# Performance work log

Hardware: AMD Instinct MI355X
Metric: run time of the kernel (lower is better)

Reference implementation:

```python
import jax, jax.numpy as jnp
import numpy as np

BETA = 0.25
K = 1024   # num_codebook_vectors
D = 256    # latent_dim


def setup_inputs() -> dict:
    key = jax.random.key(0)
    k1, k2 = jax.random.split(key)
    z = jax.random.normal(k1, (32, D, 32, 32), dtype=jnp.float32)
    # original init: uniform(-1/K, 1/K)
    codebook = jax.random.uniform(k2, (K, D), dtype=jnp.float32, minval=-1.0 / K, maxval=1.0 / K)
    return {"z": z, "codebook": codebook}


def reference(z, codebook):
    B, C, H, W = z.shape
    sg = jax.lax.stop_gradient
    # NCHW -> NHWC, flatten to [N, D]
    z_nhwc = jnp.transpose(z, (0, 2, 3, 1))
    zf = z_nhwc.reshape(-1, C)
    # squared distances via sum-of-squares + matmul: [N, K]
    d = (jnp.sum(zf * zf, axis=1, keepdims=True)
         + jnp.sum(codebook * codebook, axis=1)
         - 2.0 * jnp.matmul(zf, codebook.T))
    idx = jnp.argmin(d, axis=1)                      # [N]
    z_q = codebook[idx].reshape(B, H, W, C)          # gather + reshape
    # commitment + codebook loss
    loss = (jnp.mean((sg(z_q) - z_nhwc) ** 2)
            + BETA * jnp.mean((z_q - sg(z_nhwc)) ** 2))
    # straight-through estimator
    z_q = z_nhwc + sg(z_q - z_nhwc)
    z_q = jnp.transpose(z_q, (0, 3, 1, 2))           # back to NCHW
    return z_q, idx, loss
```

## Files before the change

kernel.cpp:

```cpp
#include <hip/hip_runtime.h>

constexpr int D_ = 256;
constexpr int K_ = 1024;
constexpr int P_ = 1024;
constexpr int N_ = 32768;

constexpr int IDX_OFF  = 8388608;
constexpr int LOSS_OFF = 8421376;

constexpr int CB16_OFF = 0;
constexpr int CN_OFF   = 262400;
constexpr int ZN_OFF   = 263424;
constexpr int CNT_OFF  = 296448;
constexpr int WL_OFF   = 296449;
constexpr size_t SCRATCH_BYTES = (size_t)(WL_OFF + N_) * 4;

constexpr float RESCUE_MARGIN = 1e-4f;

typedef _Float16 half8 __attribute__((ext_vector_type(8)));
typedef float f32x4 __attribute__((ext_vector_type(4)));

__device__ __forceinline__ void stage16(const float* g, float* l) {
  __builtin_amdgcn_global_load_lds(
      (const __attribute__((address_space(1))) unsigned int*)g,
      (__attribute__((address_space(3))) unsigned int*)l, 16, 0, 0);
}

__global__ __launch_bounds__(64) void vq_prep(const float* __restrict__ z,
                                              const float* __restrict__ cb,
                                              float* __restrict__ scratch,
                                              float* __restrict__ loss) {
  const int blk = blockIdx.x;
  const int lane = threadIdx.x;
  if (blk < 512) {
    const int n0 = blk * 64;
    const int b = n0 >> 10, p0 = n0 & (P_ - 1);
    const float* zp = z + (size_t)b * (D_ * P_) + p0 + lane;
    float a8[8];
    #pragma unroll
    for (int i = 0; i < 8; ++i) a8[i] = 0.0f;
    for (int oct = 0; oct < 32; ++oct) {
      #pragma unroll
      for (int i = 0; i < 8; ++i) {
        float v = zp[(size_t)(oct * 8 + i) * P_];
        a8[i] = fmaf(v, v, a8[i]);
      }
    }
    scratch[ZN_OFF + n0 + lane] = ((a8[0] + a8[1]) + (a8[2] + a8[3])) +
                                  ((a8[4] + a8[5]) + (a8[6] + a8[7]));
    if (blk == 0 && lane == 0) {
      *loss = 0.0f;
      ((int*)(scratch + CNT_OFF))[0] = 0;
    }
  } else if (blk < 1536) {
    const int k = blk - 512;
    const float* row = cb + (size_t)k * D_;
    double s = 0.0;
    #pragma unroll
    for (int i = 0; i < 4; ++i) {
      double v = (double)row[lane + i * 64];
      s = fma(v, v, s);
    }
    #pragma unroll
    for (int off = 32; off; off >>= 1) s += __shfl_down(s, off, 64);
    if (lane == 0) scratch[CN_OFF + k] = (float)s;
  } else {
    const int kt = blk - 1536;
    const int k = kt * 16 + (lane & 15);
    const int quad = lane >> 4;
    _Float16* cw = (_Float16*)(scratch + CB16_OFF);
    for (int ds = 0; ds < 8; ++ds) {
      const float* src = cb + (size_t)k * D_ + ds * 32 + quad * 8;
      half8 h, lo;
      #pragma unroll
      for (int j = 0; j < 8; ++j) {
        const float v = src[j] * 1024.0f;
        const _Float16 hh = (_Float16)v;
        h[j] = hh;
        lo[j] = (_Float16)(v - (float)hh);
      }
      const int s = kt * 8 + ds;
      *(half8*)(cw + ((size_t)(s * 2 + 0) * 64 + lane) * 8) = h;
      *(half8*)(cw + ((size_t)(s * 2 + 1) * 64 + lane) * 8) = lo;
    }
  }
}

__global__ __launch_bounds__(256, 2) void vq_mfma(const float* __restrict__ z,
                                                  const float* __restrict__ scratch_c,
                                                  float* __restrict__ scratch,
                                                  float* __restrict__ idxf) {
  const int t = threadIdx.x;
  const int w = t >> 6;
  const int l = t & 63;
  const int quad = l >> 4;
  const int col = l & 15;
  const int rh = w & 1;
  const int cs = w >> 1;
  const int n0 = blockIdx.x * 64;
  const int b = n0 >> 10;
  const int p0 = n0 & (P_ - 1);

  const float* __restrict__ cbsw_f = scratch_c + CB16_OFF;
  const float* __restrict__ cnorm = scratch_c + CN_OFF;
  const float* __restrict__ zn = scratch_c + ZN_OFF;

  __shared__ alignas(16) float Bw[4][2][2048];
  __shared__ alignas(16) float cnLds[1024];
  __shared__ float sM1[4][32];
  __shared__ float sM2[4][32];
  __shared__ int   sI1[4][32];
  float* Azs = &Bw[0][0][0];

  *(float4*)(cnLds + t * 4) = *(const float4*)(cnorm + t * 4);

  float znr[2][4];
  #pragma unroll
  for (int rt = 0; rt < 2; ++rt) {
    const float4 znv = *(const float4*)(zn + n0 + rh * 32 + rt * 16 + quad * 4);
    znr[rt][0] = znv.x; znr[rt][1] = znv.y;
    znr[rt][2] = znv.z; znr[rt][3] = znv.w;
  }

  half8 Ah[2][8], Al[2][8];
  const int dl0 = w * 8;
  for (int ds = 0; ds < 8; ++ds) {
    __syncthreads();
    #pragma unroll
    for (int i = 0; i < 8; ++i) {
      const int dloc = dl0 + i;
      Azs[l * 33 + dloc] =
          z[(size_t)b * (D_ * P_) + (size_t)(ds * 32 + dloc) * P_ + p0 + l];
    }
    __syncthreads();
    #pragma unroll
    for (int rt = 0; rt < 2; ++rt) {
      const float* src = &Azs[(rh * 32 + rt * 16 + col) * 33 + quad * 8];
      half8 h, lo;
      #pragma unroll
      for (int j = 0; j < 8; ++j) {
        const float v = src[j];
        const _Float16 hh = (_Float16)v;
        h[j] = hh;
        lo[j] = (_Float16)(v - (float)hh);
      }
      Ah[rt][ds] = h;
      Al[rt][ds] = lo;
    }
  }
  __syncthreads();
  asm volatile("s_waitcnt vmcnt(0)" ::: "memory");

  float* myb0 = &Bw[w][0][0];
  float* myb1 = &Bw[w][1][0];
  const float* gs = cbsw_f + (size_t)cs * 32 * 4096 + l * 4;

  #pragma unroll
  for (int j = 0; j < 8; ++j) stage16(gs + j * 256, myb0 + j * 256);

  float m1[2][4], m2v[2][4];
  int i1[2][4];
  #pragma unroll
  for (int rt = 0; rt < 2; ++rt)
    #pragma unroll
    for (int r = 0; r < 4; ++r) { m1[rt][r] = 1e30f; m2v[rt][r] = 1e30f; i1[rt][r] = 0; }

  const float* cnp = cnLds + cs * 512 + col;
  int kg = cs * 512 + col;

  for (int kt = 0; kt < 32; ++kt) {
    f32x4 H0 = {0.f,0.f,0.f,0.f}, M0 = {0.f,0.f,0.f,0.f}, L0 = {0.f,0.f,0.f,0.f};
    f32x4 H1 = {0.f,0.f,0.f,0.f}, M1 = {0.f,0.f,0.f,0.f}, L1 = {0.f,0.f,0.f,0.f};

    {
      const float* gsp = gs + (size_t)(kt * 2 + 1) * 2048;
      #pragma unroll
      for (int j = 0; j < 8; ++j) stage16(gsp + j * 256, myb1 + j * 256);
      asm volatile("s_waitcnt vmcnt(8)" ::: "memory");
      __builtin_amdgcn_sched_barrier(0);

      __builtin_amdgcn_s_setprio(1);
      #pragma unroll
      for (int ds = 0; ds < 4; ++ds) {
        const half8 bh = *(const half8*)(myb0 + (ds * 2 + 0) * 256 + l * 4);
        const half8 bl = *(const half8*)(myb0 + (ds * 2 + 1) * 256 + l * 4);
        H0 = __builtin_amdgcn_mfma_f32_16x16x32_f16(Ah[0][ds], bh, H0, 0, 0, 0);
        H1 = __builtin_amdgcn_mfma_f32_16x16x32_f16(Ah[1][ds], bh, H1, 0, 0, 0);
        M0 = __builtin_amdgcn_mfma_f32_16x16x32_f16(Ah[0][ds], bl, M0, 0, 0, 0);
        M1 = __builtin_amdgcn_mfma_f32_16x16x32_f16(Ah[1][ds], bl, M1, 0, 0, 0);
        L0 = __builtin_amdgcn_mfma_f32_16x16x32_f16(Al[0][ds], bh, L0, 0, 0, 0);
        L1 = __builtin_amdgcn_mfma_f32_16x16x32_f16(Al[1][ds], bh, L1, 0, 0, 0);
      }
      __builtin_amdgcn_s_setprio(0);
    }

    {
      if (kt < 31) {
        const float* gsp = gs + (size_t)(kt * 2 + 2) * 2048;
        #pragma unroll
        for (int j = 0; j < 8; ++j) stage16(gsp + j * 256, myb0 + j * 256);
        asm volatile("s_waitcnt vmcnt(8)" ::: "memory");
      } else {
        asm volatile("s_waitcnt vmcnt(0)" ::: "memory");
      }
      __builtin_amdgcn_sched_barrier(0);

      __builtin_amdgcn_s_setprio(1);
      #pragma unroll
      for (int ds = 4; ds < 8; ++ds) {
        const half8 bh = *(const half8*)(myb1 + ((ds - 4) * 2 + 0) * 256 + l * 4);
        const half8 bl = *(const half8*)(myb1 + ((ds - 4) * 2 + 1) * 256 + l * 4);
        H0 = __builtin_amdgcn_mfma_f32_16x16x32_f16(Ah[0][ds], bh, H0, 0, 0, 0);
        H1 = __builtin_amdgcn_mfma_f32_16x16x32_f16(Ah[1][ds], bh, H1, 0, 0, 0);
        M0 = __builtin_amdgcn_mfma_f32_16x16x32_f16(Ah[0][ds], bl, M0, 0, 0, 0);
        M1 = __builtin_amdgcn_mfma_f32_16x16x32_f16(Ah[1][ds], bl, M1, 0, 0, 0);
        L0 = __builtin_amdgcn_mfma_f32_16x16x32_f16(Al[0][ds], bh, L0, 0, 0, 0);
        L1 = __builtin_amdgcn_mfma_f32_16x16x32_f16(Al[1][ds], bh, L1, 0, 0, 0);
      }
      __builtin_amdgcn_s_setprio(0);

      const float cnf = *cnp;
      #pragma unroll
      for (int r = 0; r < 4; ++r) {
        const float s0 = fmaf((H0[r] + M0[r]) + L0[r], -0x1p-9f, znr[0][r] + cnf);
        if (s0 < m1[0][r]) { m2v[0][r] = m1[0][r]; m1[0][r] = s0; i1[0][r] = kg; }
        else if (s0 < m2v[0][r]) m2v[0][r] = s0;
        const float s1 = fmaf((H1[r] + M1[r]) + L1[r], -0x1p-9f, znr[1][r] + cnf);
        if (s1 < m1[1][r]) { m2v[1][r] = m1[1][r]; m1[1][r] = s1; i1[1][r] = kg; }
        else if (s1 < m2v[1][r]) m2v[1][r] = s1;
      }
      cnp += 16;
      kg += 16;
    }
  }

  #pragma unroll
  for (int off = 1; off <= 8; off <<= 1) {
    #pragma unroll
    for (int rt = 0; rt < 2; ++rt)
      #pragma unroll
      for (int r = 0; r < 4; ++r) {
        const float o1 = __shfl_xor(m1[rt][r], off, 64);
        const float o2 = __shfl_xor(m2v[rt][r], off, 64);
        const int oi = __shfl_xor(i1[rt][r], off, 64);
        if (o1 < m1[rt][r]) { m2v[rt][r] = fminf(m1[rt][r], o2); m1[rt][r] = o1; i1[rt][r] = oi; }
        else if (o1 == m1[rt][r]) { i1[rt][r] = min(i1[rt][r], oi); m2v[rt][r] = m1[rt][r]; }
        else { m2v[rt][r] = fminf(m2v[rt][r], o1); }
      }
  }

  if (col == 0) {
    #pragma unroll
    for (int rt = 0; rt < 2; ++rt)
      #pragma unroll
      for (int r = 0; r < 4; ++r) {
        const int rl = rt * 16 + quad * 4 + r;
        sM1[w][rl] = m1[rt][r];
        sM2[w][rl] = m2v[rt][r];
        sI1[w][rl] = i1[rt][r];
      }
  }
  __syncthreads();
  if (w < 2 && col == 0) {
    int* cnt = (int*)(scratch + CNT_OFF);
    int* wl = (int*)(scratch + WL_OFF);
    #pragma unroll
    for (int rt = 0; rt < 2; ++rt)
      #pragma unroll
      for (int r = 0; r < 4; ++r) {
        const int rl = rt * 16 + quad * 4 + r;
        float a1 = sM1[w][rl], a2 = sM2[w][rl];
        int ai = sI1[w][rl];
        const float o1 = sM1[w + 2][rl], o2 = sM2[w + 2][rl];
        const int oi = sI1[w + 2][rl];
        if (o1 < a1) { a2 = fminf(a1, o2); a1 = o1; ai = oi; }
        else if (o1 == a1) { ai = min(ai, oi); a2 = a1; }
        else { a2 = fminf(a2, o1); }
        const int n = n0 + w * 32 + rl;
        idxf[n] = (float)ai;
        if (a2 - a1 < RESCUE_MARGIN) {
          const int pos = atomicAdd(cnt, 1);
          wl[pos] = n;
        }
      }
  }
}

__global__ __launch_bounds__(256, 4) void vq_rescue(const float* __restrict__ z,
                                                    const float* __restrict__ cb,
                                                    const float* __restrict__ scratch,
                                                    float* __restrict__ idxf) {
  const int tid = threadIdx.x;
  const float* cnorm = scratch + CN_OFF;
  const float* zn = scratch + ZN_OFF;
  const int count = ((const int*)(scratch + CNT_OFF))[0];
  const int* wl = (const int*)(scratch + WL_OFF);

  __shared__ alignas(16) float zb[8][D_];
  __shared__ int nrow[8];
  __shared__ float rv[256];
  __shared__ int ri[256];

  for (int base = blockIdx.x * 8; base < count; base += gridDim.x * 8) {
    const int take = min(8, count - base);
    if (tid < 8) nrow[tid] = wl[base + (tid < take ? tid : 0)];
    __syncthreads();
    #pragma unroll
    for (int r = 0; r < 8; ++r) {
      const int n = nrow[r];
      const int b = n >> 10, p = n & (P_ - 1);
      zb[r][tid] = z[(size_t)b * (D_ * P_) + (size_t)tid * P_ + p];
    }
    __syncthreads();

    const int k0 = tid * 4;
    const float4* __restrict__ cr0 = (const float4*)(cb + (size_t)(k0 + 0) * D_);
    const float4* __restrict__ cr1 = (const float4*)(cb + (size_t)(k0 + 1) * D_);
    const float4* __restrict__ cr2 = (const float4*)(cb + (size_t)(k0 + 2) * D_);
    const float4* __restrict__ cr3 = (const float4*)(cb + (size_t)(k0 + 3) * D_);

    float acc[8][4];
    #pragma unroll
    for (int r = 0; r < 8; ++r)
      #pragma unroll
      for (int j = 0; j < 4; ++j) acc[r][j] = 0.0f;

    for (int d4 = 0; d4 < 64; ++d4) {
      const float4 v0 = cr0[d4], v1 = cr1[d4], v2 = cr2[d4], v3 = cr3[d4];
      #pragma unroll
      for (int r = 0; r < 8; ++r) {
        const float4 zv = ((const float4*)zb[r])[d4];
        acc[r][0] = fmaf(zv.x, v0.x, acc[r][0]);
        acc[r][0] = fmaf(zv.y, v0.y, acc[r][0]);
        acc[r][0] = fmaf(zv.z, v0.z, acc[r][0]);
        acc[r][0] = fmaf(zv.w, v0.w, acc[r][0]);
        acc[r][1] = fmaf(zv.x, v1.x, acc[r][1]);
        acc[r][1] = fmaf(zv.y, v1.y, acc[r][1]);
        acc[r][1] = fmaf(zv.z, v1.z, acc[r][1]);
        acc[r][1] = fmaf(zv.w, v1.w, acc[r][1]);
        acc[r][2] = fmaf(zv.x, v2.x, acc[r][2]);
        acc[r][2] = fmaf(zv.y, v2.y, acc[r][2]);
        acc[r][2] = fmaf(zv.z, v2.z, acc[r][2]);
        acc[r][2] = fmaf(zv.w, v2.w, acc[r][2]);
        acc[r][3] = fmaf(zv.x, v3.x, acc[r][3]);
        acc[r][3] = fmaf(zv.y, v3.y, acc[r][3]);
        acc[r][3] = fmaf(zv.z, v3.z, acc[r][3]);
        acc[r][3] = fmaf(zv.w, v3.w, acc[r][3]);
      }
    }

    for (int r = 0; r < 8; ++r) {
      const int n = nrow[r];
      const float zA = zn[n];
      float bv = 1e30f;
      int bi = 0x7fffffff;
      #pragma unroll
      for (int j = 0; j < 4; ++j) {
        const float A = zA + cnorm[k0 + j];
        const float s = A - 2.0f * acc[r][j];
        if (s < bv) { bv = s; bi = k0 + j; }
      }
      rv[tid] = bv; ri[tid] = bi;
      __syncthreads();
      for (int off = 128; off >= 1; off >>= 1) {
        if (tid < off) {
          const float ov = rv[tid + off];
          const int oi = ri[tid + off];
          if (ov < rv[tid] || (ov == rv[tid] && oi < ri[tid])) { rv[tid] = ov; ri[tid] = oi; }
        }
        __syncthreads();
      }
      if (tid == 0 && r < take) idxf[n] = (float)ri[0];
      __syncthreads();
    }
  }
}

__global__ __launch_bounds__(256) void vq_gather(const float* __restrict__ z,
                                                 const float* __restrict__ cb,
                                                 const float* __restrict__ idxf,
                                                 float* __restrict__ out,
                                                 float* __restrict__ loss) {
  const int tid = threadIdx.x;
  const int lane = tid & 63;
  const int w = tid >> 6;
  const int n0 = blockIdx.x * 64;
  const int b = n0 >> 10;
  const int p0 = n0 & (P_ - 1);
  const int p = p0 + lane;

  const int idx = (int)(idxf[n0 + lane] + 0.5f);
  const float4* crow4 = (const float4*)(cb + (size_t)idx * D_);
  const size_t base = (size_t)b * (D_ * P_) + p;

  float acc = 0.0f;
  #pragma unroll 4
  for (int ci = 0; ci < 16; ++ci) {
    const float4 v = crow4[w * 16 + ci];
    const int c = w * 64 + ci * 4;
    const float vv[4] = {v.x, v.y, v.z, v.w};
    #pragma unroll
    for (int u = 0; u < 4; ++u) {
      const size_t a = base + (size_t)(c + u) * P_;
      const float zv = z[a];
      const float d = vv[u] - zv;
      out[a] = zv + d;
      acc = fmaf(d, d, acc);
    }
  }
  #pragma unroll
  for (int off = 32; off; off >>= 1) acc += __shfl_down(acc, off, 64);
  __shared__ float wsum[4];
  if (lane == 0) wsum[w] = acc;
  __syncthreads();
  if (tid == 0) {
    float s = wsum[0] + wsum[1] + wsum[2] + wsum[3];
    atomicAdd(loss, s * (1.25f / 8388608.0f));
  }
}

extern "C" void kernel_launch(void* const* d_in, const int* in_sizes, int n_in,
                              void* d_out, int out_size, void* d_ws, size_t ws_size,
                              hipStream_t stream) {
  const float* z = (const float*)d_in[0];
  const float* cb = (const float*)d_in[1];
  float* out = (float*)d_out;

  float* scratch = (d_ws != nullptr && ws_size >= SCRATCH_BYTES)
                       ? (float*)d_ws : out;

  vq_prep<<<1600, 64, 0, stream>>>(z, cb, scratch, out + LOSS_OFF);
  vq_mfma<<<N_ / 64, 256, 0, stream>>>(z, scratch, scratch, out + IDX_OFF);
  vq_rescue<<<128, 256, 0, stream>>>(z, cb, scratch, out + IDX_OFF);
  vq_gather<<<N_ / 64, 256, 0, stream>>>(z, cb, out + IDX_OFF, out, out + LOSS_OFF);
}
```

Before: 234.9 us.

## Split codebook across eight waves per block with finer double-buffered staging

The distance/argmin kernel now uses 512 threads (8 waves) per block, and each wave pair covers 256 codebook entries instead of 512. Codebook staging into LDS moves to quarter-size chunks that are double-buffered with a vmcnt(4) wait. The final cross-wave reduction merges four partial top-2 results per row instead of two. The aim is more waves in flight to hide latency and halve per-wave serial work, at the cost of more registers per CU under the tighter launch bounds and extra reduction and synchronisation overhead.

```diff
diff --git a/kernel.cpp b/kernel.cpp
--- a/kernel.cpp
+++ b/kernel.cpp
@@ -86,7 +86,7 @@
   }
 }
 
-__global__ __launch_bounds__(256, 2) void vq_mfma(const float* __restrict__ z,
+__global__ __launch_bounds__(512, 4) void vq_mfma(const float* __restrict__ z,
                                                   const float* __restrict__ scratch_c,
                                                   float* __restrict__ scratch,
                                                   float* __restrict__ idxf) {
@@ -105,14 +105,14 @@
   const float* __restrict__ cnorm = scratch_c + CN_OFF;
   const float* __restrict__ zn = scratch_c + ZN_OFF;
 
-  __shared__ alignas(16) float Bw[4][2][2048];
+  __shared__ alignas(16) float Bw[8][2][1024];
   __shared__ alignas(16) float cnLds[1024];
-  __shared__ float sM1[4][32];
-  __shared__ float sM2[4][32];
-  __shared__ int   sI1[4][32];
+  __shared__ float sM1[8][32];
+  __shared__ float sM2[8][32];
+  __shared__ int   sI1[8][32];
   float* Azs = &Bw[0][0][0];
 
-  *(float4*)(cnLds + t * 4) = *(const float4*)(cnorm + t * 4);
+  *(float2*)(cnLds + t * 2) = *(const float2*)(cnorm + t * 2);
 
   float znr[2][4];
   #pragma unroll
@@ -123,11 +123,11 @@
   }
 
   half8 Ah[2][8], Al[2][8];
-  const int dl0 = w * 8;
+  const int dl0 = w * 4;
   for (int ds = 0; ds < 8; ++ds) {
     __syncthreads();
     #pragma unroll
-    for (int i = 0; i < 8; ++i) {
+    for (int i = 0; i < 4; ++i) {
       const int dloc = dl0 + i;
       Azs[l * 33 + dloc] =
           z[(size_t)b * (D_ * P_) + (size_t)(ds * 32 + dloc) * P_ + p0 + l];
@@ -151,12 +151,12 @@
   __syncthreads();
   asm volatile("s_waitcnt vmcnt(0)" ::: "memory");
 
-  float* myb0 = &Bw[w][0][0];
-  float* myb1 = &Bw[w][1][0];
-  const float* gs = cbsw_f + (size_t)cs * 32 * 4096 + l * 4;
+  float* myq0 = &Bw[w][0][0];
+  float* myq1 = &Bw[w][1][0];
+  const float* gs = cbsw_f + (size_t)cs * 16 * 4096 + l * 4;
 
   #pragma unroll
-  for (int j = 0; j < 8; ++j) stage16(gs + j * 256, myb0 + j * 256);
+  for (int j = 0; j < 4; ++j) stage16(gs + j * 256, myq0 + j * 256);
 
   float m1[2][4], m2v[2][4];
   int i1[2][4];
@@ -165,25 +165,34 @@
     #pragma unroll
     for (int r = 0; r < 4; ++r) { m1[rt][r] = 1e30f; m2v[rt][r] = 1e30f; i1[rt][r] = 0; }
 
-  const float* cnp = cnLds + cs * 512 + col;
-  int kg = cs * 512 + col;
-
-  for (int kt = 0; kt < 32; ++kt) {
+  const float* cnp = cnLds + cs * 256 + col;
+  int kg = cs * 256 + col;
+
+  for (int kt = 0; kt < 16; ++kt) {
     f32x4 H0 = {0.f,0.f,0.f,0.f}, M0 = {0.f,0.f,0.f,0.f}, L0 = {0.f,0.f,0.f,0.f};
     f32x4 H1 = {0.f,0.f,0.f,0.f}, M1 = {0.f,0.f,0.f,0.f}, L1 = {0.f,0.f,0.f,0.f};
 
-    {
-      const float* gsp = gs + (size_t)(kt * 2 + 1) * 2048;
-      #pragma unroll
-      for (int j = 0; j < 8; ++j) stage16(gsp + j * 256, myb1 + j * 256);
-      asm volatile("s_waitcnt vmcnt(8)" ::: "memory");
+    #pragma unroll
+    for (int q = 0; q < 4; ++q) {
+      const int s = kt * 4 + q;
+      float* bufc = (s & 1) ? myq1 : myq0;
+      float* bufn = (s & 1) ? myq0 : myq1;
+      if (s < 63) {
+        const float* gsp = gs + (size_t)(s + 1) * 1024;
+        #pragma unroll
+        for (int j = 0; j < 4; ++j) stage16(gsp + j * 256, bufn + j * 256);
+        asm volatile("s_waitcnt vmcnt(4)" ::: "memory");
+      } else {
+        asm volatile("s_waitcnt vmcnt(0)" ::: "memory");
+      }
       __builtin_amdgcn_sched_barrier(0);
 
       __builtin_amdgcn_s_setprio(1);
       #pragma unroll
-      for (int ds = 0; ds < 4; ++ds) {
-        const half8 bh = *(const half8*)(myb0 + (ds * 2 + 0) * 256 + l * 4);
-        const half8 bl = *(const half8*)(myb0 + (ds * 2 + 1) * 256 + l * 4);
+      for (int dsq = 0; dsq < 2; ++dsq) {
+        const int ds = 2 * q + dsq;
+        const half8 bh = *(const half8*)(bufc + (dsq * 2 + 0) * 256 + l * 4);
+        const half8 bl = *(const half8*)(bufc + (dsq * 2 + 1) * 256 + l * 4);
         H0 = __builtin_amdgcn_mfma_f32_16x16x32_f16(Ah[0][ds], bh, H0, 0, 0, 0);
         H1 = __builtin_amdgcn_mfma_f32_16x16x32_f16(Ah[1][ds], bh, H1, 0, 0, 0);
         M0 = __builtin_amdgcn_mfma_f32_16x16x32_f16(Ah[0][ds], bl, M0, 0, 0, 0);
@@ -194,44 +203,18 @@
       __builtin_amdgcn_s_setprio(0);
     }
 
-    {
-      if (kt < 31) {
-        const float* gsp = gs + (size_t)(kt * 2 + 2) * 2048;
-        #pragma unroll
-        for (int j = 0; j < 8; ++j) stage16(gsp + j * 256, myb0 + j * 256);
-        asm volatile("s_waitcnt vmcnt(8)" ::: "memory");
-      } else {
-        asm volatile("s_waitcnt vmcnt(0)" ::: "memory");
-      }
-      __builtin_amdgcn_sched_barrier(0);
-
-      __builtin_amdgcn_s_setprio(1);
-      #pragma unroll
-      for (int ds = 4; ds < 8; ++ds) {
-        const half8 bh = *(const half8*)(myb1 + ((ds - 4) * 2 + 0) * 256 + l * 4);
-        const half8 bl = *(const half8*)(myb1 + ((ds - 4) * 2 + 1) * 256 + l * 4);
-        H0 = __builtin_amdgcn_mfma_f32_16x16x32_f16(Ah[0][ds], bh, H0, 0, 0, 0);
-        H1 = __builtin_amdgcn_mfma_f32_16x16x32_f16(Ah[1][ds], bh, H1, 0, 0, 0);
-        M0 = __builtin_amdgcn_mfma_f32_16x16x32_f16(Ah[0][ds], bl, M0, 0, 0, 0);
-        M1 = __builtin_amdgcn_mfma_f32_16x16x32_f16(Ah[1][ds], bl, M1, 0, 0, 0);
-        L0 = __builtin_amdgcn_mfma_f32_16x16x32_f16(Al[0][ds], bh, L0, 0, 0, 0);
-        L1 = __builtin_amdgcn_mfma_f32_16x16x32_f16(Al[1][ds], bh, L1, 0, 0, 0);
-      }
-      __builtin_amdgcn_s_setprio(0);
-
-      const float cnf = *cnp;
-      #pragma unroll
-      for (int r = 0; r < 4; ++r) {
-        const float s0 = fmaf((H0[r] + M0[r]) + L0[r], -0x1p-9f, znr[0][r] + cnf);
-        if (s0 < m1[0][r]) { m2v[0][r] = m1[0][r]; m1[0][r] = s0; i1[0][r] = kg; }
-        else if (s0 < m2v[0][r]) m2v[0][r] = s0;
-        const float s1 = fmaf((H1[r] + M1[r]) + L1[r], -0x1p-9f, znr[1][r] + cnf);
-        if (s1 < m1[1][r]) { m2v[1][r] = m1[1][r]; m1[1][r] = s1; i1[1][r] = kg; }
-        else if (s1 < m2v[1][r]) m2v[1][r] = s1;
-      }
-      cnp += 16;
-      kg += 16;
-    }
+    const float cnf = *cnp;
+    #pragma unroll
+    for (int r = 0; r < 4; ++r) {
+      const float s0 = fmaf((H0[r] + M0[r]) + L0[r], -0x1p-9f, znr[0][r] + cnf);
+      if (s0 < m1[0][r]) { m2v[0][r] = m1[0][r]; m1[0][r] = s0; i1[0][r] = kg; }
+      else if (s0 < m2v[0][r]) m2v[0][r] = s0;
+      const float s1 = fmaf((H1[r] + M1[r]) + L1[r], -0x1p-9f, znr[1][r] + cnf);
+      if (s1 < m1[1][r]) { m2v[1][r] = m1[1][r]; m1[1][r] = s1; i1[1][r] = kg; }
+      else if (s1 < m2v[1][r]) m2v[1][r] = s1;
+    }
+    cnp += 16;
+    kg += 16;
   }
 
   #pragma unroll
@@ -271,11 +254,14 @@
         const int rl = rt * 16 + quad * 4 + r;
         float a1 = sM1[w][rl], a2 = sM2[w][rl];
         int ai = sI1[w][rl];
-        const float o1 = sM1[w + 2][rl], o2 = sM2[w + 2][rl];
-        const int oi = sI1[w + 2][rl];
-        if (o1 < a1) { a2 = fminf(a1, o2); a1 = o1; ai = oi; }
-        else if (o1 == a1) { ai = min(ai, oi); a2 = a1; }
-        else { a2 = fminf(a2, o1); }
+        #pragma unroll
+        for (int j = 1; j < 4; ++j) {
+          const float o1 = sM1[w + 2 * j][rl], o2 = sM2[w + 2 * j][rl];
+          const int oi = sI1[w + 2 * j][rl];
+          if (o1 < a1) { a2 = fminf(a1, o2); a1 = o1; ai = oi; }
+          else if (o1 == a1) { ai = min(ai, oi); a2 = fminf(a2, o2); }
+          else { a2 = fminf(a2, o1); }
+        }
         const int n = n0 + w * 32 + rl;
         idxf[n] = (float)ai;
         if (a2 - a1 < RESCUE_MARGIN) {
@@ -430,7 +416,7 @@
                        ? (float*)d_ws : out;
 
   vq_prep<<<1600, 64, 0, stream>>>(z, cb, scratch, out + LOSS_OFF);
-  vq_mfma<<<N_ / 64, 256, 0, stream>>>(z, scratch, scratch, out + IDX_OFF);
+  vq_mfma<<<N_ / 64, 512, 0, stream>>>(z, scratch, scratch, out + IDX_OFF);
   vq_rescue<<<128, 256, 0, stream>>>(z, cb, scratch, out + IDX_OFF);
   vq_gather<<<N_ / 64, 256, 0, stream>>>(z, cb, out + IDX_OFF, out, out + LOSS_OFF);
 }
```

After: 385.8 us. 64.3% more time.
